# Optimization experiments

Measured on AMD Instinct MI355X. Metric: run time of the kernel, lower is better.

The kernel has to match this reference:

```python
import jax, jax.numpy as jnp
import numpy as np

N_NODES = 50000
N_EDGES = 800000
IN_CH = 256
OUT_CH = 64  # heads=1
NEG_SLOPE = 0.2


def setup_inputs() -> dict:
    key = jax.random.key(0)
    k1, k2, k3, k4, k5 = jax.random.split(key, 5)
    x = jax.random.normal(k1, (N_NODES, IN_CH), dtype=jnp.float32)
    edge_index = jax.random.randint(k2, (2, N_EDGES), 0, N_NODES, dtype=jnp.int64)
    # glorot init for dense weight [out, in] (torch Linear layout) and att [out, 2]
    s_w = np.sqrt(6.0 / (OUT_CH + IN_CH)).astype(np.float32)
    W = jax.random.uniform(k3, (OUT_CH, IN_CH), minval=-s_w, maxval=s_w, dtype=jnp.float32)
    b = jnp.zeros((OUT_CH,), dtype=jnp.float32)
    s_a = np.sqrt(6.0 / (OUT_CH + 2)).astype(np.float32)
    att = jax.random.uniform(k4, (OUT_CH, 2), minval=-s_a, maxval=s_a, dtype=jnp.float32)
    return {"x": x, "edge_index": edge_index, "W": W, "b": b, "att": att}


def reference(x, edge_index, W, b, att):
    n = x.shape[0]
    # dense projection: feature [N, OUT_CH]
    feature = x @ W.T + b
    # per-node attention contributions: e_pre [N, 2]
    e_pre = feature @ att
    tar = edge_index[0]  # flow='target_to_source'
    src = edge_index[1]
    # edge logit = leakyrelu(a_tar(t) + a_src(s)); self-loop logit per node
    logit_edge = jax.nn.leaky_relu(e_pre[tar, 0] + e_pre[src, 1], NEG_SLOPE)
    logit_self = jax.nn.leaky_relu(e_pre[:, 0] + e_pre[:, 1], NEG_SLOPE)
    # segment softmax over {self edge} U {incoming edges} per target node
    m = jnp.maximum(jax.ops.segment_max(logit_edge, tar, num_segments=n), logit_self)
    exp_edge = jnp.exp(logit_edge - m[tar])
    exp_self = jnp.exp(logit_self - m)
    denom = exp_self + jax.ops.segment_sum(exp_edge, tar, num_segments=n)
    alpha = exp_edge / denom[tar]          # [E]
    alpha_self = exp_self / denom          # [N]
    # weighted gather-scatter aggregation (fused_gas_agg)
    msgs = alpha[:, None] * feature[src]   # [E, OUT_CH]
    out = alpha_self[:, None] * feature + jax.ops.segment_sum(msgs, tar, num_segments=n)
    return out
```

## Files before the change

kernel.cpp:

```cpp
#include <hip/hip_runtime.h>
#include <math.h>

#define N_NODES 50000
#define N_EDGES 800000
#define IN_CH 256
#define OUT_CH 64
#define NEG_SLOPE 0.2f
#define PAD 64

typedef __bf16 bf16x4 __attribute__((ext_vector_type(4)));
typedef __bf16 bf16x8 __attribute__((ext_vector_type(8)));
typedef float  f32x4  __attribute__((ext_vector_type(4)));

__global__ __launch_bounds__(256) void k_gemm(
    const float* __restrict__ x, const float* __restrict__ W,
    const float* __restrict__ bias, const float* __restrict__ att,
    __bf16* __restrict__ featb, float* __restrict__ e0,
    float* __restrict__ e1, int* __restrict__ deg)
{
    __shared__ __bf16 A[64][72];
    __shared__ __bf16 B[64][72];

    const int t    = threadIdx.x;
    const int row0 = blockIdx.x * 64;
    const int wv   = t >> 6;
    const int li   = t & 63;
    const int lm   = li & 15;
    const int lq   = li >> 4;

    if (t < 64 && row0 + t < N_NODES) deg[row0 + t] = 0;

    f32x4 acc[4];
    #pragma unroll
    for (int tn = 0; tn < 4; ++tn) acc[tn] = (f32x4){0.f, 0.f, 0.f, 0.f};

    const int sr = t >> 2;
    const int cq = t & 3;
    const int gr = row0 + sr;
    const bool ok = (gr < N_NODES);

    for (int kc = 0; kc < IN_CH; kc += 64) {
        __syncthreads();
        #pragma unroll
        for (int i = 0; i < 4; ++i) {
            int kk = cq * 16 + i * 4;
            float4 v = make_float4(0.f, 0.f, 0.f, 0.f);
            if (ok)
                v = *reinterpret_cast<const float4*>(&x[(size_t)gr * IN_CH + kc + kk]);
            bf16x4 h = {(__bf16)v.x, (__bf16)v.y, (__bf16)v.z, (__bf16)v.w};
            *reinterpret_cast<bf16x4*>(&A[sr][kk]) = h;

            float4 w1 = *reinterpret_cast<const float4*>(&W[(size_t)sr * IN_CH + kc + kk]);
            bf16x4 g = {(__bf16)w1.x, (__bf16)w1.y, (__bf16)w1.z, (__bf16)w1.w};
            *reinterpret_cast<bf16x4*>(&B[sr][kk]) = g;
        }
        __syncthreads();

        #pragma unroll
        for (int half = 0; half < 2; ++half) {
            int ko = half * 32 + lq * 8;
            bf16x8 a = *reinterpret_cast<const bf16x8*>(&A[wv * 16 + lm][ko]);
            #pragma unroll
            for (int tn = 0; tn < 4; ++tn) {
                bf16x8 b = *reinterpret_cast<const bf16x8*>(&B[tn * 16 + lm][ko]);
                acc[tn] = __builtin_amdgcn_mfma_f32_16x16x32_bf16(a, b, acc[tn], 0, 0, 0);
            }
        }
    }

    float att0[4], att1[4], bv[4];
    #pragma unroll
    for (int tn = 0; tn < 4; ++tn) {
        int c = tn * 16 + lm;
        att0[tn] = att[c * 2 + 0];
        att1[tn] = att[c * 2 + 1];
        bv[tn]   = bias[c];
    }

    float p0[4] = {0.f, 0.f, 0.f, 0.f};
    float p1[4] = {0.f, 0.f, 0.f, 0.f};
    #pragma unroll
    for (int r = 0; r < 4; ++r) {
        int row = row0 + wv * 16 + lq * 4 + r;
        #pragma unroll
        for (int tn = 0; tn < 4; ++tn) {
            float f = acc[tn][r] + bv[tn];
            if (row < N_NODES)
                featb[(size_t)row * OUT_CH + tn * 16 + lm] = (__bf16)f;
            p0[r] += f * att0[tn];
            p1[r] += f * att1[tn];
        }
    }

    #pragma unroll
    for (int m = 1; m < 16; m <<= 1) {
        #pragma unroll
        for (int r = 0; r < 4; ++r) {
            p0[r] += __shfl_xor(p0[r], m, 64);
            p1[r] += __shfl_xor(p1[r], m, 64);
        }
    }
    if (lm == 0) {
        #pragma unroll
        for (int r = 0; r < 4; ++r) {
            int row = row0 + wv * 16 + lq * 4 + r;
            if (row < N_NODES) {
                e0[row] = p0[r];
                e1[row] = p1[r];
            }
        }
    }
}

__global__ __launch_bounds__(256) void k_hist(
    const int* __restrict__ ei, int* __restrict__ deg,
    unsigned short* __restrict__ e_slot)
{
    int e = blockIdx.x * blockDim.x + threadIdx.x;
    if (e >= N_EDGES) return;
    e_slot[e] = (unsigned short)atomicAdd(&deg[ei[e]], 1);
}

__global__ __launch_bounds__(256) void k_fill(
    const int* __restrict__ ei, const unsigned short* __restrict__ e_slot,
    unsigned short* __restrict__ pcsr)
{
    int e = blockIdx.x * blockDim.x + threadIdx.x;
    if (e >= N_EDGES) return;
    int tnode = ei[e];
    int snode = ei[N_EDGES + e];
    int slot = (int)e_slot[e];
    if (slot < PAD)
        pcsr[(size_t)tnode * PAD + slot] = (unsigned short)snode;
}

__global__ __launch_bounds__(256) void k_gather(
    const float* __restrict__ e0, const float* __restrict__ e1,
    const __bf16* __restrict__ featb, const int* __restrict__ deg,
    const unsigned short* __restrict__ pcsr, float* __restrict__ out)
{
    int t    = blockIdx.x * 4 + (threadIdx.x >> 6);
    int lane = threadIdx.x & 63;
    if (t >= N_NODES) return;

    int cnt = deg[t];
    cnt = cnt > PAD ? PAD : cnt;

    float e0t = e0[t];

    int   si = (int)pcsr[(size_t)t * PAD + lane];
    float qi = e1[si];
    float zi = e0t + qi;
    float wi_raw = __expf(zi > 0.f ? zi : NEG_SLOPE * zi);
    float wi = (lane < cnt) ? wi_raw : 0.f;

    float zs  = e0t + e1[t];
    float wsf = __expf(zs > 0.f ? zs : NEG_SLOPE * zs);

    float wsum = wi;
    #pragma unroll
    for (int m = 1; m < 64; m <<= 1)
        wsum += __shfl_xor(wsum, m, 64);
    wsum += wsf;

    float acc = wsf * (float)featb[(size_t)t * OUT_CH + lane];

    int i = 0;
    for (; i + 4 <= cnt; i += 4) {
        int   s0 = __shfl(si, i,     64), s1 = __shfl(si, i + 1, 64);
        int   s2 = __shfl(si, i + 2, 64), s3 = __shfl(si, i + 3, 64);
        float w0 = __shfl(wi, i,     64), w1 = __shfl(wi, i + 1, 64);
        float w2 = __shfl(wi, i + 2, 64), w3 = __shfl(wi, i + 3, 64);
        float f0 = (float)featb[(size_t)s0 * OUT_CH + lane];
        float f1 = (float)featb[(size_t)s1 * OUT_CH + lane];
        float f2 = (float)featb[(size_t)s2 * OUT_CH + lane];
        float f3 = (float)featb[(size_t)s3 * OUT_CH + lane];
        acc += w0 * f0 + w1 * f1 + w2 * f2 + w3 * f3;
    }
    for (; i < cnt; ++i) {
        int   s0 = __shfl(si, i, 64);
        float w0 = __shfl(wi, i, 64);
        acc += w0 * (float)featb[(size_t)s0 * OUT_CH + lane];
    }

    out[(size_t)t * OUT_CH + lane] = acc / wsum;
}

extern "C" void kernel_launch(void* const* d_in, const int* in_sizes, int n_in,
                              void* d_out, int out_size, void* d_ws, size_t ws_size,
                              hipStream_t stream)
{
    const float* x    = (const float*)d_in[0];
    const int*   ei   = (const int*)d_in[1];
    const float* W    = (const float*)d_in[2];
    const float* bias = (const float*)d_in[3];
    const float* att  = (const float*)d_in[4];
    float* out = (float*)d_out;

    __bf16* featb = (__bf16*)d_ws;
    float*  e0    = (float*)(featb + (size_t)N_NODES * OUT_CH);
    float*  e1    = e0 + N_NODES;
    int*    deg   = (int*)(e1 + N_NODES);
    unsigned short* pcsr   = (unsigned short*)(deg + N_NODES);
    unsigned short* e_slot = pcsr + (size_t)N_NODES * PAD;

    dim3 blk(256);

    k_gemm<<<dim3((N_NODES + 63) / 64), blk, 0, stream>>>(
        x, W, bias, att, featb, e0, e1, deg);

    k_hist<<<dim3((N_EDGES + 255) / 256), blk, 0, stream>>>(ei, deg, e_slot);

    k_fill<<<dim3((N_EDGES + 255) / 256), blk, 0, stream>>>(ei, e_slot, pcsr);

    k_gather<<<dim3((N_NODES + 3) / 4), blk, 0, stream>>>(
        e0, e1, featb, deg, pcsr, out);
}
```

Before: 179.5 us.

## Pad degree counters to separate cache lines and stream x directly into MFMA

```diff
diff --git a/kernel.cpp b/kernel.cpp
--- a/kernel.cpp
+++ b/kernel.cpp
@@ -7,6 +7,7 @@
 #define OUT_CH 64
 #define NEG_SLOPE 0.2f
 #define PAD 64
+#define DEGS 16
 
 typedef __bf16 bf16x4 __attribute__((ext_vector_type(4)));
 typedef __bf16 bf16x8 __attribute__((ext_vector_type(8)));
@@ -18,8 +19,7 @@
     __bf16* __restrict__ featb, float* __restrict__ e0,
     float* __restrict__ e1, int* __restrict__ deg)
 {
-    __shared__ __bf16 A[64][72];
-    __shared__ __bf16 B[64][72];
+    __shared__ __bf16 B[64][264];
 
     const int t    = threadIdx.x;
     const int row0 = blockIdx.x * 64;
@@ -28,43 +28,51 @@
     const int lm   = li & 15;
     const int lq   = li >> 4;
 
-    if (t < 64 && row0 + t < N_NODES) deg[row0 + t] = 0;
+    {
+        int idx = row0 * DEGS + t * 4;
+        if (idx + 3 < N_NODES * DEGS)
+            *reinterpret_cast<int4*>(&deg[idx]) = make_int4(0, 0, 0, 0);
+        else {
+            #pragma unroll
+            for (int j = 0; j < 4; ++j)
+                if (idx + j < N_NODES * DEGS) deg[idx + j] = 0;
+        }
+    }
+
+    {
+        const int sr = t >> 2;
+        const int cq = t & 3;
+        #pragma unroll
+        for (int j = 0; j < 4; ++j) {
+            #pragma unroll
+            for (int i = 0; i < 4; ++i) {
+                int kk = j * 64 + cq * 16 + i * 4;
+                float4 w1 = *reinterpret_cast<const float4*>(&W[(size_t)sr * IN_CH + kk]);
+                bf16x4 g = {(__bf16)w1.x, (__bf16)w1.y, (__bf16)w1.z, (__bf16)w1.w};
+                *reinterpret_cast<bf16x4*>(&B[sr][kk]) = g;
+            }
+        }
+    }
+    __syncthreads();
+
+    const int myrow = row0 + wv * 16 + lm;
+    const float* xrow = x + (size_t)(myrow < N_NODES ? myrow : 0) * IN_CH;
 
     f32x4 acc[4];
     #pragma unroll
     for (int tn = 0; tn < 4; ++tn) acc[tn] = (f32x4){0.f, 0.f, 0.f, 0.f};
 
-    const int sr = t >> 2;
-    const int cq = t & 3;
-    const int gr = row0 + sr;
-    const bool ok = (gr < N_NODES);
-
-    for (int kc = 0; kc < IN_CH; kc += 64) {
-        __syncthreads();
-        #pragma unroll
-        for (int i = 0; i < 4; ++i) {
-            int kk = cq * 16 + i * 4;
-            float4 v = make_float4(0.f, 0.f, 0.f, 0.f);
-            if (ok)
-                v = *reinterpret_cast<const float4*>(&x[(size_t)gr * IN_CH + kc + kk]);
-            bf16x4 h = {(__bf16)v.x, (__bf16)v.y, (__bf16)v.z, (__bf16)v.w};
-            *reinterpret_cast<bf16x4*>(&A[sr][kk]) = h;
-
-            float4 w1 = *reinterpret_cast<const float4*>(&W[(size_t)sr * IN_CH + kc + kk]);
-            bf16x4 g = {(__bf16)w1.x, (__bf16)w1.y, (__bf16)w1.z, (__bf16)w1.w};
-            *reinterpret_cast<bf16x4*>(&B[sr][kk]) = g;
-        }
-        __syncthreads();
-
-        #pragma unroll
-        for (int half = 0; half < 2; ++half) {
-            int ko = half * 32 + lq * 8;
-            bf16x8 a = *reinterpret_cast<const bf16x8*>(&A[wv * 16 + lm][ko]);
-            #pragma unroll
-            for (int tn = 0; tn < 4; ++tn) {
-                bf16x8 b = *reinterpret_cast<const bf16x8*>(&B[tn * 16 + lm][ko]);
-                acc[tn] = __builtin_amdgcn_mfma_f32_16x16x32_bf16(a, b, acc[tn], 0, 0, 0);
-            }
+    #pragma unroll
+    for (int kb = 0; kb < 8; ++kb) {
+        int ko = kb * 32 + lq * 8;
+        float4 a0 = *reinterpret_cast<const float4*>(&xrow[ko]);
+        float4 a1 = *reinterpret_cast<const float4*>(&xrow[ko + 4]);
+        bf16x8 a = {(__bf16)a0.x, (__bf16)a0.y, (__bf16)a0.z, (__bf16)a0.w,
+                    (__bf16)a1.x, (__bf16)a1.y, (__bf16)a1.z, (__bf16)a1.w};
+        #pragma unroll
+        for (int tn = 0; tn < 4; ++tn) {
+            bf16x8 b = *reinterpret_cast<const bf16x8*>(&B[tn * 16 + lm][ko]);
+            acc[tn] = __builtin_amdgcn_mfma_f32_16x16x32_bf16(a, b, acc[tn], 0, 0, 0);
         }
     }
 
@@ -118,7 +126,7 @@
 {
     int e = blockIdx.x * blockDim.x + threadIdx.x;
     if (e >= N_EDGES) return;
-    e_slot[e] = (unsigned short)atomicAdd(&deg[ei[e]], 1);
+    e_slot[e] = (unsigned short)atomicAdd(&deg[ei[e] * DEGS], 1);
 }
 
 __global__ __launch_bounds__(256) void k_fill(
@@ -143,7 +151,7 @@
     int lane = threadIdx.x & 63;
     if (t >= N_NODES) return;
 
-    int cnt = deg[t];
+    int cnt = deg[t * DEGS];
     cnt = cnt > PAD ? PAD : cnt;
 
     float e0t = e0[t];
@@ -201,7 +209,7 @@
     float*  e0    = (float*)(featb + (size_t)N_NODES * OUT_CH);
     float*  e1    = e0 + N_NODES;
     int*    deg   = (int*)(e1 + N_NODES);
-    unsigned short* pcsr   = (unsigned short*)(deg + N_NODES);
+    unsigned short* pcsr   = (unsigned short*)(deg + (size_t)N_NODES * DEGS);
     unsigned short* e_slot = pcsr + (size_t)N_NODES * PAD;
 
     dim3 blk(256);
```

New measurement: 173.4 us. -3.4%, faster.
